# Performance work log

Measured on AMD Instinct MI355X. Metric: run time of the kernel, lower is better.

## Reference

```python
import jax, jax.numpy as jnp
import numpy as np

GRID_SIZE = 5
SPLINE_ORDER = 3
GRID_LO, GRID_HI = -1.0, 1.0
N_COEFF = GRID_SIZE + SPLINE_ORDER  # 8


def make_grid(in_features):
    # (in_features, grid_size + 2*spline_order + 1) = (in, 12)
    h = (GRID_HI - GRID_LO) / GRID_SIZE
    g = jnp.arange(-SPLINE_ORDER, GRID_SIZE + SPLINE_ORDER + 1, dtype=jnp.float32) * h + GRID_LO
    return jnp.broadcast_to(g, (in_features, g.shape[0]))


def b_splines(x, grid):
    # x: (N, in); grid: (in, G). Returns (N, in, grid_size+spline_order).
    xe = x[..., None]
    bases = ((xe >= grid[:, :-1]) & (xe < grid[:, 1:])).astype(x.dtype)
    for k in range(1, SPLINE_ORDER + 1):
        left = (xe - grid[:, :-(k + 1)]) / (grid[:, k:-1] - grid[:, :-(k + 1)]) * bases[..., :-1]
        right = (grid[:, k + 1:] - xe) / (grid[:, k + 1:] - grid[:, 1:-k]) * bases[..., 1:]
        bases = left + right
    return bases


def kan_linear(x, base_w, spline_w, scaler, grid):
    # base branch: SiLU(x) @ base_w^T
    base_out = jax.nn.silu(x) @ base_w.T
    # spline branch: basis (N,in,c) contracted with scaled spline weight (out,in,c)
    b = b_splines(x, grid)
    sw = spline_w * scaler[..., None]
    spline_out = jnp.einsum('nic,oic->no', b, sw)
    return base_out + spline_out


def setup_inputs() -> dict:
    key = jax.random.key(0)
    ks = jax.random.split(key, 7)
    d_model, d_hid = 512, 2049  # d_ff + 1
    s = 0.1  # keep activations roughly inside grid range
    return {
        "x": jax.random.normal(ks[0], (4096, d_model), dtype=jnp.float32) * 0.3,
        "base_w1": jax.random.normal(ks[1], (d_hid, d_model), dtype=jnp.float32) * s,
        "spline_w1": jax.random.normal(ks[2], (d_hid, d_model, N_COEFF), dtype=jnp.float32) * s,
        "scaler1": jax.random.normal(ks[3], (d_hid, d_model), dtype=jnp.float32) * s,
        "base_w2": jax.random.normal(ks[4], (d_model, d_hid), dtype=jnp.float32) * s,
        "spline_w2": jax.random.normal(ks[5], (d_model, d_hid, N_COEFF), dtype=jnp.float32) * s,
        "scaler2": jax.random.normal(ks[6], (d_model, d_hid), dtype=jnp.float32) * s,
    }


def reference(x, base_w1, spline_w1, scaler1, base_w2, spline_w2, scaler2):
    grid1 = make_grid(x.shape[-1])
    h = kan_linear(x, base_w1, spline_w1, scaler1, grid1)
    grid2 = make_grid(h.shape[-1])
    out = kan_linear(h, base_w2, spline_w2, scaler2, grid2)
    return out
```

## Files before the change

kernel.cpp:

```cpp
#include <hip/hip_runtime.h>
#include <hip/hip_bf16.h>

#define T_TOK 4096
#define I1    512
#define O1    2049
#define K1    4608
#define NG1   576
#define I2    2049
#define O2    512
#define K2    18560
#define NG2   2320
#define N1G   2048
#define HPART ((size_t)T_TOK * N1G)

typedef __attribute__((ext_vector_type(8))) short short8;
typedef __attribute__((ext_vector_type(4))) float floatx4;
typedef __attribute__((address_space(3))) void* lds_ptr_t;
typedef const __attribute__((address_space(1))) void* gmem_ptr_t;

__device__ __forceinline__ unsigned short f2bf(float f) {
  union { __hip_bfloat16 h; unsigned short u; } cv;
  cv.h = __float2bfloat16(f);
  return cv.u;
}
__device__ __forceinline__ float b2f(unsigned short u) {
  union { float f; unsigned u; } c; c.u = (unsigned)u << 16; return c.f;
}
__device__ __forceinline__ unsigned bfr(float f) {
  union { float f; unsigned u; } c; c.f = f;
  return (c.u + 0x8000u) >> 16;
}
__device__ __forceinline__ float silu_f(float x) { return x / (1.0f + __expf(-x)); }

__device__ __forceinline__ uint4 spline_pack(float h) {
  float u = (h + 2.2f) * 2.5f;
  int ji = (int)u;
  ji = ji < 0 ? 0 : (ji > 10 ? 10 : ji);
  float t = u - (float)ji;
  float it = 1.0f - t, t2 = t * t, t3 = t2 * t;
  float b0 = it * it * it * (1.0f / 6.0f);
  float b1 = (3.0f * t3 - 6.0f * t2 + 4.0f) * (1.0f / 6.0f);
  float b2 = (-3.0f * t3 + 3.0f * t2 + 3.0f * t + 1.0f) * (1.0f / 6.0f);
  float b3 = t3 * (1.0f / 6.0f);
  unsigned pk01 = bfr(b0) | (bfr(b1) << 16);
  unsigned pk23 = bfr(b2) | (bfr(b3) << 16);
  unsigned long long p64 = (unsigned long long)pk01 | ((unsigned long long)pk23 << 32);
  bool inR = (h >= -2.2f) && (h < 2.2f);
  p64 = inR ? p64 : 0ull;
  int sh = (ji - 3) * 16;
  int shr = sh < 0 ? -sh : 0;
  int shl = sh < 0 ? 0 : sh;
  __uint128_t v = ((__uint128_t)(p64 >> shr)) << shl;
  union { __uint128_t q; uint4 u4; } cv;
  cv.q = v;
  return cv.u4;
}

__global__ void pack_w1_kernel(const float* __restrict__ bw, const float* __restrict__ sw,
                               const float* __restrict__ sc, unsigned short* __restrict__ W) {
  int k = blockIdx.x * 256 + threadIdx.x;
  int o = blockIdx.y;
  float v;
  if (k < 4096) v = sw[(size_t)o * 4096 + k] * sc[(size_t)o * I1 + (k >> 3)];
  else          v = bw[(size_t)o * I1 + (k - 4096)];
  W[(size_t)o * K1 + k] = f2bf(v);
}

__global__ void pack_w2_kernel(const float* __restrict__ bw, const float* __restrict__ sw,
                               const float* __restrict__ sc, unsigned short* __restrict__ W) {
  int k = blockIdx.x * 256 + threadIdx.x;
  if (k >= K2) return;
  int o = blockIdx.y;
  float v = 0.0f;
  if (k < 16392)      v = sw[(size_t)o * 16392 + k] * sc[(size_t)o * I2 + (k >> 3)];
  else if (k < 18441) v = bw[(size_t)o * I2 + (k - 16392)];
  W[(size_t)o * K2 + k] = f2bf(v);
}

__global__ void expand1_kernel(const float* __restrict__ x, unsigned short* __restrict__ A) {
  int g = blockIdx.x * 256 + threadIdx.x;
  if (g >= NG1) return;
  int m = blockIdx.y;
  uint4 val;
  if (g < 512) {
    val = spline_pack(x[(size_t)m * I1 + g]);
  } else {
    const float4* xr = (const float4*)(x + (size_t)m * I1 + (size_t)(g - 512) * 8);
    float4 a = xr[0], b = xr[1];
    union { unsigned short s[8]; uint4 v; } pk;
    pk.s[0] = f2bf(silu_f(a.x)); pk.s[1] = f2bf(silu_f(a.y));
    pk.s[2] = f2bf(silu_f(a.z)); pk.s[3] = f2bf(silu_f(a.w));
    pk.s[4] = f2bf(silu_f(b.x)); pk.s[5] = f2bf(silu_f(b.y));
    pk.s[6] = f2bf(silu_f(b.z)); pk.s[7] = f2bf(silu_f(b.w));
    val = pk.v;
  }
  *(uint4*)(A + (size_t)m * K1 + (size_t)g * 8) = val;
}

__global__ void gemv_col_kernel(const unsigned short* __restrict__ A1,
                                const unsigned short* __restrict__ W1,
                                float* __restrict__ Hcol) {
  int m = blockIdx.x * 4 + (threadIdx.x >> 6);
  int lane = threadIdx.x & 63;
  const unsigned short* a  = A1 + (size_t)m * K1;
  const unsigned short* wr = W1 + (size_t)2048 * K1;
  float s = 0.0f;
#pragma unroll
  for (int c = 0; c < 9; ++c) {
    int off = (c * 64 + lane) * 8;
    short8 av = *(const short8*)(a + off);
    short8 wv = *(const short8*)(wr + off);
#pragma unroll
    for (int j = 0; j < 8; ++j)
      s += b2f((unsigned short)av[j]) * b2f((unsigned short)wv[j]);
  }
#pragma unroll
  for (int d = 32; d >= 1; d >>= 1) s += __shfl_down(s, d);
  if (lane == 0) Hcol[m] = s;
}

__global__ void expand2_kernel(const float* __restrict__ Ha, const float* __restrict__ Hb,
                               const float* __restrict__ Hcol, unsigned short* __restrict__ A) {
  int g = blockIdx.x * 256 + threadIdx.x;
  if (g >= NG2) return;
  int m = blockIdx.y;
  float hc = Hcol[m];
  uint4 val;
  if (g < 2049) {
    float h = (g < N1G) ? Ha[(size_t)m * N1G + g] + Hb[(size_t)m * N1G + g] : hc;
    val = spline_pack(h);
  } else if (g < 2306) {
    int c0 = (g - 2049) * 8;
    union { unsigned short s[8]; uint4 v; } pk;
#pragma unroll
    for (int c = 0; c < 8; ++c) {
      int idx = c0 + c;
      float v = 0.0f;
      if (idx < I2) {
        float h = (idx < N1G) ? Ha[(size_t)m * N1G + idx] + Hb[(size_t)m * N1G + idx] : hc;
        v = silu_f(h);
      }
      pk.s[c] = f2bf(v);
    }
    val = pk.v;
  } else {
    val = make_uint4(0u, 0u, 0u, 0u);
  }
  *(uint4*)(A + (size_t)m * K2 + (size_t)g * 8) = val;
}

__device__ __forceinline__ void BARv() { asm volatile("s_barrier" ::: "memory"); }
__device__ __forceinline__ void LGKM0() {
  asm volatile("s_waitcnt lgkmcnt(0)" ::: "memory");
  __builtin_amdgcn_sched_barrier(0);
}
__device__ __forceinline__ void VM0() { asm volatile("s_waitcnt vmcnt(0)" ::: "memory"); }

__device__ __forceinline__ void read_af(short8* af, const unsigned short* Asp,
                                        int wmh, int mh, int kk, int q, int ln) {
#pragma unroll
  for (int j = 0; j < 4; ++j) {
    int rr = wmh * 128 + (mh * 4 + j) * 16 + ln;
    int cl = (kk * 4 + q) ^ (rr & 7);
    af[j] = *(const short8*)&Asp[rr * 64 + cl * 8];
  }
}
__device__ __forceinline__ void read_bf(short8* bf, const unsigned short* Bsp,
                                        int wnq, int kk, int q, int ln) {
#pragma unroll
  for (int n = 0; n < 4; ++n) {
    int rb = wnq * 64 + n * 16 + ln;
    int cl = (kk * 4 + q) ^ (rb & 7);
    bf[n] = *(const short8*)&Bsp[rb * 64 + cl * 8];
  }
}

__global__ __launch_bounds__(512, 2)
void gemm256_kernel(const unsigned short* __restrict__ Aw, const unsigned short* __restrict__ Bw,
                    float* __restrict__ C, int Ktot, int kStep, int nBx, int nBz,
                    int ldc, size_t pslice, int storeMode)
{
  __shared__ __align__(16) unsigned short As[2][256 * 64];
  __shared__ __align__(16) unsigned short Bs[2][256 * 64];

  const int Lb = blockIdx.x;
  const int wgid = (Lb & 7) * 32 + (Lb >> 3);
  const int bx = wgid % nBx;
  const int tq = wgid / nBx;
  const int by = tq & 15;
  const int bz = tq >> 4;

  const int tid = threadIdx.x;
  const int ks = bz * kStep;
  const int ke = (bz == nBz - 1) ? Ktot : ks + kStep;
  const int ntiles = (ke - ks) >> 6;

  const int w = tid >> 6, L = tid & 63, q = L >> 4, ln = L & 15;
  const int wmh = w & 1;
  const int wnq = w >> 1;

  floatx4 zf = {0.f, 0.f, 0.f, 0.f};
  floatx4 acc[8][4];
#pragma unroll
  for (int f = 0; f < 8; ++f)
#pragma unroll
    for (int n = 0; n < 4; ++n)
      acc[f][n] = zf;

  const unsigned short* gA[4];
  const unsigned short* gB[4];
  int ldsO[4];
#pragma unroll
  for (int l = 0; l < 4; ++l) {
    int e = l * 512 + tid;
    int br = e >> 3;
    int cg = (e & 7) ^ (br & 7);
    gA[l] = Aw + ((size_t)(by * 256 + br)) * Ktot + ks + cg * 8;
    gB[l] = Bw + ((size_t)(bx * 256 + br)) * Ktot + ks + cg * 8;
    ldsO[l] = e * 8;
  }

  {
    unsigned short* Asn = (unsigned short*)As[0];
    unsigned short* Bsn = (unsigned short*)Bs[0];
#pragma unroll
    for (int l = 0; l < 4; ++l) {
      __builtin_amdgcn_global_load_lds((gmem_ptr_t)gA[l], (lds_ptr_t)&Asn[ldsO[l]], 16, 0, 0);
      gA[l] += 64;
      __builtin_amdgcn_global_load_lds((gmem_ptr_t)gB[l], (lds_ptr_t)&Bsn[ldsO[l]], 16, 0, 0);
      gB[l] += 64;
    }
  }
  VM0(); BARv();

  for (int t = 0; t < ntiles; ++t) {
    unsigned short* Asp = (unsigned short*)As[t & 1];
    unsigned short* Bsp = (unsigned short*)Bs[t & 1];
    unsigned short* Asn = (unsigned short*)As[(t & 1) ^ 1];
    unsigned short* Bsn = (unsigned short*)Bs[(t & 1) ^ 1];
    const bool pf = (t + 1 < ntiles);
    short8 af[4], bf[4];

    read_bf(bf, Bsp, wnq, 0, q, ln);
    read_af(af, Asp, wmh, 0, 0, q, ln);
    if (pf) {
#pragma unroll
      for (int l = 0; l < 4; ++l) {
        __builtin_amdgcn_global_load_lds((gmem_ptr_t)gA[l], (lds_ptr_t)&Asn[ldsO[l]], 16, 0, 0);
        gA[l] += 64;
      }
    }
    BARv(); LGKM0();
    __builtin_amdgcn_s_setprio(1);
#pragma unroll
    for (int j = 0; j < 4; ++j)
#pragma unroll
      for (int n = 0; n < 4; ++n)
        acc[j][n] = __builtin_amdgcn_mfma_f32_16x16x32_bf16(af[j], bf[n], acc[j][n], 0, 0, 0);
    __builtin_amdgcn_s_setprio(0);
    BARv();

    read_af(af, Asp, wmh, 1, 0, q, ln);
    if (pf) {
#pragma unroll
      for (int l = 0; l < 4; ++l) {
        __builtin_amdgcn_global_load_lds((gmem_ptr_t)gB[l], (lds_ptr_t)&Bsn[ldsO[l]], 16, 0, 0);
        gB[l] += 64;
      }
    }
    BARv(); LGKM0();
    __builtin_amdgcn_s_setprio(1);
#pragma unroll
    for (int j = 0; j < 4; ++j)
#pragma unroll
      for (int n = 0; n < 4; ++n)
        acc[4 + j][n] = __builtin_amdgcn_mfma_f32_16x16x32_bf16(af[j], bf[n], acc[4 + j][n], 0, 0, 0);
    __builtin_amdgcn_s_setprio(0);
    BARv();

    read_bf(bf, Bsp, wnq, 1, q, ln);
    read_af(af, Asp, wmh, 0, 1, q, ln);
    BARv(); LGKM0();
    __builtin_amdgcn_s_setprio(1);
#pragma unroll
    for (int j = 0; j < 4; ++j)
#pragma unroll
      for (int n = 0; n < 4; ++n)
        acc[j][n] = __builtin_amdgcn_mfma_f32_16x16x32_bf16(af[j], bf[n], acc[j][n], 0, 0, 0);
    __builtin_amdgcn_s_setprio(0);
    BARv();

    read_af(af, Asp, wmh, 1, 1, q, ln);
    BARv(); LGKM0();
    __builtin_amdgcn_s_setprio(1);
#pragma unroll
    for (int j = 0; j < 4; ++j)
#pragma unroll
      for (int n = 0; n < 4; ++n)
        acc[4 + j][n] = __builtin_amdgcn_mfma_f32_16x16x32_bf16(af[j], bf[n], acc[4 + j][n], 0, 0, 0);
    __builtin_amdgcn_s_setprio(0);
    VM0();
    BARv();
  }

  const int gmb = by * 256 + wmh * 128 + q * 4;
  const int gnb = bx * 256 + wnq * 64 + ln;
  if (storeMode == 0) {
    float* Cp = C + (size_t)bz * pslice;
#pragma unroll
    for (int f = 0; f < 8; ++f)
#pragma unroll
      for (int n = 0; n < 4; ++n)
#pragma unroll
        for (int rg = 0; rg < 4; ++rg)
          Cp[(size_t)(gmb + f * 16 + rg) * ldc + (gnb + n * 16)] = acc[f][n][rg];
  } else {
#pragma unroll
    for (int f = 0; f < 8; ++f)
#pragma unroll
      for (int n = 0; n < 4; ++n)
#pragma unroll
        for (int rg = 0; rg < 4; ++rg)
          atomicAdd(&C[(size_t)(gmb + f * 16 + rg) * ldc + (gnb + n * 16)], acc[f][n][rg]);
  }
}

extern "C" void kernel_launch(void* const* d_in, const int* in_sizes, int n_in,
                              void* d_out, int out_size, void* d_ws, size_t ws_size,
                              hipStream_t stream) {
  const float* x   = (const float*)d_in[0];
  const float* bw1 = (const float*)d_in[1];
  const float* sw1 = (const float*)d_in[2];
  const float* sc1 = (const float*)d_in[3];
  const float* bw2 = (const float*)d_in[4];
  const float* sw2 = (const float*)d_in[5];
  const float* sc2 = (const float*)d_in[6];
  float* out = (float*)d_out;

  float* Ha = (float*)d_ws;
  float* Hb = Ha + HPART;
  float* Hcol = Hb + HPART;
  unsigned short* W2 = (unsigned short*)(Hcol + 16384);
  unsigned short* A2 = W2 + (size_t)O2 * K2;
  unsigned short* A1 = A2;
  unsigned short* W1 = A1 + (size_t)T_TOK * K1;

  hipMemsetAsync(d_out, 0, (size_t)out_size * sizeof(float), stream);

  pack_w1_kernel<<<dim3(K1 / 256, O1), 256, 0, stream>>>(bw1, sw1, sc1, W1);
  pack_w2_kernel<<<dim3((K2 + 255) / 256, O2), 256, 0, stream>>>(bw2, sw2, sc2, W2);
  expand1_kernel<<<dim3((NG1 + 255) / 256, T_TOK), 256, 0, stream>>>(x, A1);

  gemv_col_kernel<<<T_TOK / 4, 256, 0, stream>>>(A1, W1, Hcol);

  gemm256_kernel<<<256, 512, 0, stream>>>(A1, W1, Ha, K1, 2304, 8, 2, N1G, HPART, 0);

  expand2_kernel<<<dim3((NG2 + 255) / 256, T_TOK), 256, 0, stream>>>(Ha, Hb, Hcol, A2);

  gemm256_kernel<<<256, 512, 0, stream>>>(A2, W2, out, K2, 2304, 2, 8, O2, 0, 2);
}
```

Before: 435.3 us.

## Use 4-stage LDS ring with K=32 tiles and one barrier per tile

Restructures the bf16 MFMA GEMM main loop. The two-buffer, K=64 scheme had four barrier/wait phases per tile; the new loop uses a four-slot ring of K=32 tiles and keeps three tiles of global-to-LDS loads in flight. Each slot stores the 256-row tile as two 128-row halves with an XOR swizzle, and fragment offsets are precomputed. Each iteration then needs only one partial vmcnt wait and one barrier, which should hide more memory latency and cut synchronisation cost. The trade-off is less MFMA work per barrier and more fragment registers live at once.

After: 461.2 us. +6.0%, slower.

```diff
diff --git a/kernel.cpp b/kernel.cpp
--- a/kernel.cpp
+++ b/kernel.cpp
@@ -149,39 +149,13 @@
   *(uint4*)(A + (size_t)m * K2 + (size_t)g * 8) = val;
 }
 
-__device__ __forceinline__ void BARv() { asm volatile("s_barrier" ::: "memory"); }
-__device__ __forceinline__ void LGKM0() {
-  asm volatile("s_waitcnt lgkmcnt(0)" ::: "memory");
-  __builtin_amdgcn_sched_barrier(0);
-}
-__device__ __forceinline__ void VM0() { asm volatile("s_waitcnt vmcnt(0)" ::: "memory"); }
-
-__device__ __forceinline__ void read_af(short8* af, const unsigned short* Asp,
-                                        int wmh, int mh, int kk, int q, int ln) {
-#pragma unroll
-  for (int j = 0; j < 4; ++j) {
-    int rr = wmh * 128 + (mh * 4 + j) * 16 + ln;
-    int cl = (kk * 4 + q) ^ (rr & 7);
-    af[j] = *(const short8*)&Asp[rr * 64 + cl * 8];
-  }
-}
-__device__ __forceinline__ void read_bf(short8* bf, const unsigned short* Bsp,
-                                        int wnq, int kk, int q, int ln) {
-#pragma unroll
-  for (int n = 0; n < 4; ++n) {
-    int rb = wnq * 64 + n * 16 + ln;
-    int cl = (kk * 4 + q) ^ (rb & 7);
-    bf[n] = *(const short8*)&Bsp[rb * 64 + cl * 8];
-  }
-}
-
 __global__ __launch_bounds__(512, 2)
 void gemm256_kernel(const unsigned short* __restrict__ Aw, const unsigned short* __restrict__ Bw,
                     float* __restrict__ C, int Ktot, int kStep, int nBx, int nBz,
                     int ldc, size_t pslice, int storeMode)
 {
-  __shared__ __align__(16) unsigned short As[2][256 * 64];
-  __shared__ __align__(16) unsigned short Bs[2][256 * 64];
+  __shared__ __align__(16) unsigned short As[4][8192];
+  __shared__ __align__(16) unsigned short Bs[4][8192];
 
   const int Lb = blockIdx.x;
   const int wgid = (Lb & 7) * 32 + (Lb >> 3);
@@ -193,7 +167,7 @@
   const int tid = threadIdx.x;
   const int ks = bz * kStep;
   const int ke = (bz == nBz - 1) ? Ktot : ks + kStep;
-  const int ntiles = (ke - ks) >> 6;
+  const int ntiles = (ke - ks) >> 5;
 
   const int w = tid >> 6, L = tid & 63, q = L >> 4, ln = L & 15;
   const int wmh = w & 1;
@@ -207,100 +181,78 @@
     for (int n = 0; n < 4; ++n)
       acc[f][n] = zf;
 
-  const unsigned short* gA[4];
-  const unsigned short* gB[4];
-  int ldsO[4];
-#pragma unroll
-  for (int l = 0; l < 4; ++l) {
+  const unsigned short* gA[2];
+  const unsigned short* gB[2];
+  int ldsO[2];
+#pragma unroll
+  for (int l = 0; l < 2; ++l) {
     int e = l * 512 + tid;
-    int br = e >> 3;
-    int cg = (e & 7) ^ (br & 7);
-    gA[l] = Aw + ((size_t)(by * 256 + br)) * Ktot + ks + cg * 8;
-    gB[l] = Bw + ((size_t)(bx * 256 + br)) * Ktot + ks + cg * 8;
+    int rr = e >> 3, j = e & 7, jj = j ^ (rr & 7);
+    int trow = ((jj >> 2) << 7) + rr, tcg = jj & 3;
+    gA[l] = Aw + (size_t)(by * 256 + trow) * Ktot + ks + tcg * 8;
+    gB[l] = Bw + (size_t)(bx * 256 + trow) * Ktot + ks + tcg * 8;
     ldsO[l] = e * 8;
   }
 
-  {
-    unsigned short* Asn = (unsigned short*)As[0];
-    unsigned short* Bsn = (unsigned short*)Bs[0];
-#pragma unroll
-    for (int l = 0; l < 4; ++l) {
-      __builtin_amdgcn_global_load_lds((gmem_ptr_t)gA[l], (lds_ptr_t)&Asn[ldsO[l]], 16, 0, 0);
-      gA[l] += 64;
-      __builtin_amdgcn_global_load_lds((gmem_ptr_t)gB[l], (lds_ptr_t)&Bsn[ldsO[l]], 16, 0, 0);
-      gB[l] += 64;
+#pragma unroll
+  for (int tt = 0; tt < 3; ++tt) {
+#pragma unroll
+    for (int l = 0; l < 2; ++l) {
+      __builtin_amdgcn_global_load_lds((gmem_ptr_t)(gA[l] + tt * 32), (lds_ptr_t)&As[tt][ldsO[l]], 16, 0, 0);
+      __builtin_amdgcn_global_load_lds((gmem_ptr_t)(gB[l] + tt * 32), (lds_ptr_t)&Bs[tt][ldsO[l]], 16, 0, 0);
     }
   }
-  VM0(); BARv();
+#pragma unroll
+  for (int l = 0; l < 2; ++l) { gA[l] += 96; gB[l] += 96; }
+  asm volatile("s_waitcnt vmcnt(8)" ::: "memory");
+  asm volatile("s_barrier" ::: "memory");
+
+  int aoff[8], boff[4];
+#pragma unroll
+  for (int f = 0; f < 8; ++f) {
+    int r = f * 16 + ln;
+    aoff[f] = r * 64 + (((q + (wmh << 2)) ^ (r & 7)) << 3);
+  }
+#pragma unroll
+  for (int n = 0; n < 4; ++n) {
+    int rb = wnq * 64 + n * 16 + ln;
+    int r = rb & 127;
+    boff[n] = r * 64 + (((q + ((wnq >> 1) << 2)) ^ (r & 7)) << 3);
+  }
 
   for (int t = 0; t < ntiles; ++t) {
-    unsigned short* Asp = (unsigned short*)As[t & 1];
-    unsigned short* Bsp = (unsigned short*)Bs[t & 1];
-    unsigned short* Asn = (unsigned short*)As[(t & 1) ^ 1];
-    unsigned short* Bsn = (unsigned short*)Bs[(t & 1) ^ 1];
-    const bool pf = (t + 1 < ntiles);
-    short8 af[4], bf[4];
-
-    read_bf(bf, Bsp, wnq, 0, q, ln);
-    read_af(af, Asp, wmh, 0, 0, q, ln);
-    if (pf) {
-#pragma unroll
-      for (int l = 0; l < 4; ++l) {
-        __builtin_amdgcn_global_load_lds((gmem_ptr_t)gA[l], (lds_ptr_t)&Asn[ldsO[l]], 16, 0, 0);
-        gA[l] += 64;
+    const unsigned short* Asp = As[t & 3];
+    const unsigned short* Bsp = Bs[t & 3];
+    if (t + 3 < ntiles) {
+      int sn = (t + 3) & 3;
+#pragma unroll
+      for (int l = 0; l < 2; ++l) {
+        __builtin_amdgcn_global_load_lds((gmem_ptr_t)gA[l], (lds_ptr_t)&As[sn][ldsO[l]], 16, 0, 0);
+        gA[l] += 32;
+        __builtin_amdgcn_global_load_lds((gmem_ptr_t)gB[l], (lds_ptr_t)&Bs[sn][ldsO[l]], 16, 0, 0);
+        gB[l] += 32;
       }
     }
-    BARv(); LGKM0();
+    __builtin_amdgcn_sched_barrier(0);
+
+    short8 af[8], bf[4];
+#pragma unroll
+    for (int f = 0; f < 8; ++f) af[f] = *(const short8*)&Asp[aoff[f]];
+#pragma unroll
+    for (int n = 0; n < 4; ++n) bf[n] = *(const short8*)&Bsp[boff[n]];
+
     __builtin_amdgcn_s_setprio(1);
 #pragma unroll
-    for (int j = 0; j < 4; ++j)
+    for (int f = 0; f < 8; ++f)
 #pragma unroll
       for (int n = 0; n < 4; ++n)
-        acc[j][n] = __builtin_amdgcn_mfma_f32_16x16x32_bf16(af[j], bf[n], acc[j][n], 0, 0, 0);
+        acc[f][n] = __builtin_amdgcn_mfma_f32_16x16x32_bf16(af[f], bf[n], acc[f][n], 0, 0, 0);
     __builtin_amdgcn_s_setprio(0);
-    BARv();
-
-    read_af(af, Asp, wmh, 1, 0, q, ln);
-    if (pf) {
-#pragma unroll
-      for (int l = 0; l < 4; ++l) {
-        __builtin_amdgcn_global_load_lds((gmem_ptr_t)gB[l], (lds_ptr_t)&Bsn[ldsO[l]], 16, 0, 0);
-        gB[l] += 64;
-      }
-    }
-    BARv(); LGKM0();
-    __builtin_amdgcn_s_setprio(1);
-#pragma unroll
-    for (int j = 0; j < 4; ++j)
-#pragma unroll
-      for (int n = 0; n < 4; ++n)
-        acc[4 + j][n] = __builtin_amdgcn_mfma_f32_16x16x32_bf16(af[j], bf[n], acc[4 + j][n], 0, 0, 0);
-    __builtin_amdgcn_s_setprio(0);
-    BARv();
-
-    read_bf(bf, Bsp, wnq, 1, q, ln);
-    read_af(af, Asp, wmh, 0, 1, q, ln);
-    BARv(); LGKM0();
-    __builtin_amdgcn_s_setprio(1);
-#pragma unroll
-    for (int j = 0; j < 4; ++j)
-#pragma unroll
-      for (int n = 0; n < 4; ++n)
-        acc[j][n] = __builtin_amdgcn_mfma_f32_16x16x32_bf16(af[j], bf[n], acc[j][n], 0, 0, 0);
-    __builtin_amdgcn_s_setprio(0);
-    BARv();
-
-    read_af(af, Asp, wmh, 1, 1, q, ln);
-    BARv(); LGKM0();
-    __builtin_amdgcn_s_setprio(1);
-#pragma unroll
-    for (int j = 0; j < 4; ++j)
-#pragma unroll
-      for (int n = 0; n < 4; ++n)
-        acc[4 + j][n] = __builtin_amdgcn_mfma_f32_16x16x32_bf16(af[j], bf[n], acc[4 + j][n], 0, 0, 0);
-    __builtin_amdgcn_s_setprio(0);
-    VM0();
-    BARv();
+
+    if (t + 3 < ntiles)       asm volatile("s_waitcnt vmcnt(8)" ::: "memory");
+    else if (t + 3 == ntiles) asm volatile("s_waitcnt vmcnt(4)" ::: "memory");
+    else                      asm volatile("s_waitcnt vmcnt(0)" ::: "memory");
+    asm volatile("s_barrier" ::: "memory");
   }
 
   const int gmb = by * 256 + wmh * 128 + q * 4;
```
